# Optimization experiments

Measured on AMD Instinct MI355X. Metric: run time of the kernel, lower is better.

Reference implementation:

```python
import jax, jax.numpy as jnp
import numpy as np

DECAY = 0.8
EPS = 1e-05


def setup_inputs() -> dict:
    key = jax.random.key(0)
    k1, k2, k3 = jax.random.split(key, 3)
    b, n, d = 16, 4096, 64
    h, c = 1, 2048
    x = jax.random.normal(k1, (b, n, d), dtype=jnp.float32)
    embeddings = jax.random.normal(k2, (h, c, d), dtype=jnp.float32)
    cluster_size = jnp.ones((h, c), dtype=jnp.float32)
    embed_avg = jax.random.normal(k3, (h, c, d), dtype=jnp.float32)
    return {"x": x, "embeddings": embeddings, "cluster_size": cluster_size, "embed_avg": embed_avg}


def reference(x, embeddings, cluster_size, embed_avg):
    # x: (b, n, d); add codebook dim h=1 and flatten -> (h, N, d)
    d = x.shape[-1]
    flat = x.reshape(1, -1, d)                              # (h, N, d)
    h, C = embeddings.shape[0], embeddings.shape[1]

    # dist = -cdist(flat, embeddings)  (negative euclidean distance)
    x2 = jnp.sum(flat * flat, axis=-1, keepdims=True)       # (h, N, 1)
    e2 = jnp.sum(embeddings * embeddings, axis=-1)          # (h, C)
    xe = jnp.einsum('hnd,hcd->hnc', flat, embeddings)       # (h, N, C)
    dist = -jnp.sqrt(jnp.clip(x2 + e2[:, None, :] - 2.0 * xe, 0.0))

    # gumbel_sample with stochastic=False, straight_through=False -> hard argmax
    embed_ind = jnp.argmax(dist, axis=-1)                   # (h, N)

    # quantize: gather selected codes
    quantize = jnp.take_along_axis(embeddings, embed_ind[..., None], axis=1)  # (h, N, d)

    # EMA codebook update (scatter-based): counts and per-code feature sums
    counts = jax.vmap(lambda i: jnp.bincount(i, length=C))(embed_ind).astype(x.dtype)  # (h, C)
    embed_sum = jax.vmap(lambda f, i: jax.ops.segment_sum(f, i, num_segments=C))(flat, embed_ind)  # (h, C, d)

    new_cluster_size = cluster_size * DECAY + counts * (1.0 - DECAY)
    new_embed_avg = embed_avg * DECAY + embed_sum * (1.0 - DECAY)

    # laplace smoothing of cluster sizes, then renormalize embed_avg
    tot = jnp.sum(new_cluster_size, axis=-1, keepdims=True)
    smoothed = (new_cluster_size + EPS) / (tot + C * EPS) * tot
    new_embeddings = new_embed_avg / smoothed[..., None]

    quantize = quantize.reshape(x.shape)                    # drop h dim back to (b, n, d)
    embed_ind = embed_ind.reshape(x.shape[:-1])             # (b, n)
    return quantize, embed_ind, new_embeddings, new_cluster_size, new_embed_avg
```

## Files before the change

kernel.cpp:

```cpp
#include <hip/hip_runtime.h>

#define N_TOK 65536
#define D 64
#define C_CODES 2048
#define DECAYF 0.8f
#define OMDF 0.2f
#define EPSF 1e-5f
#define SEG 16
#define GAP_THR 0.0625f
#define TCODES 64
#define HT (1024 / TCODES)

#define OUT_QUANT 0
#define OUT_IND   (N_TOK * D)
#define OUT_EMB   (OUT_IND + N_TOK)
#define OUT_CS    (OUT_EMB + C_CODES * D)
#define OUT_EAVG  (OUT_CS + C_CODES)

typedef short s16x8 __attribute__((ext_vector_type(8)));
typedef float f32x4 __attribute__((ext_vector_type(4)));

__device__ __forceinline__ unsigned short f2bf(float f) {
    unsigned int u = __float_as_uint(f);
    return (unsigned short)((u + 0x7fffu + ((u >> 16) & 1u)) >> 16);
}
__device__ __forceinline__ float bf2f(unsigned short h) {
    return __uint_as_float(((unsigned int)h) << 16);
}
__device__ __forceinline__ unsigned long long shflx64w(unsigned long long v, int mask, int w) {
    unsigned int lo = (unsigned int)v, hi = (unsigned int)(v >> 32);
    lo = __shfl_xor(lo, mask, w);
    hi = __shfl_xor(hi, mask, w);
    return ((unsigned long long)hi << 32) | lo;
}
__device__ __forceinline__ void gload_lds16(const void* g, void* l) {
    __builtin_amdgcn_global_load_lds(
        (const __attribute__((address_space(1))) void*)g,
        (__attribute__((address_space(3))) void*)l, 16, 0, 0);
}

__global__ void eprep_kernel(const float* __restrict__ emb, short* __restrict__ ebk,
                             float* __restrict__ e2, unsigned int* __restrict__ e2p,
                             float* __restrict__ counts, float* __restrict__ embed_sum) {
    int g = blockIdx.x * blockDim.x + threadIdx.x;
    int code = g >> 3, slot = g & 7;
    int kc = slot ^ (code & 7);
    const float4* ep = (const float4*)(emb + (size_t)code * D + kc * 8);
    float4 a = ep[0], b = ep[1];
    float v[8] = {a.x, a.y, a.z, a.w, b.x, b.y, b.z, b.w};
    s16x8 h, l;
#pragma unroll
    for (int j = 0; j < 8; ++j) {
        unsigned short hb = f2bf(v[j]);
        h[j] = (short)hb;
        l[j] = (short)f2bf(v[j] - bf2f(hb));
    }
    *(s16x8*)(ebk + (size_t)code * 128 + slot * 8) = h;
    *(s16x8*)(ebk + (size_t)code * 128 + 64 + slot * 8) = l;

    float4 z = {0.f, 0.f, 0.f, 0.f};
    ((float4*)embed_sum)[g * 2] = z;
    ((float4*)embed_sum)[g * 2 + 1] = z;
    if (g < C_CODES / 4) ((float4*)counts)[g] = z;

    if (g < C_CODES) {
        const float4* er = (const float4*)(emb + (size_t)g * D);
        float s0 = 0.f, s1 = 0.f, s2 = 0.f, s3 = 0.f;
#pragma unroll
        for (int i = 0; i < D / 4; ++i) {
            float4 e = er[i];
            s0 = fmaf(e.x, e.x, s0);
            s1 = fmaf(e.y, e.y, s1);
            s2 = fmaf(e.z, e.z, s2);
            s3 = fmaf(e.w, e.w, s3);
        }
        float vv = (s0 + s1) + (s2 + s3);
        e2[g] = vv;
        unsigned short hb = f2bf(vv);
        unsigned short lb = f2bf(vv - bf2f(hb));
        e2p[g] = (unsigned int)hb | ((unsigned int)lb << 16);
    }
}

__global__ __launch_bounds__(256) void screen_kernel(
        const float* __restrict__ x, const short* __restrict__ ebk,
        const unsigned int* __restrict__ e2p, uint4* __restrict__ ktop2,
        float* __restrict__ kb3) {
    __shared__ unsigned int e2pl[1024];
    __shared__ __align__(16) char bstage[2][TCODES * 256];

    const int tid = threadIdx.x;
    const int bh = blockIdx.y;
    ((uint4*)e2pl)[tid] = ((const uint4*)(e2p + bh * 1024))[tid];

    const int lane = tid & 63;
    const int wave = tid >> 6;
    const int col = lane & 15;
    const int krow = lane >> 4;

    s16x8 ah[2][2], al[2][2];
#pragma unroll
    for (int s = 0; s < 2; ++s) {
        int tok = blockIdx.x * 128 + wave * 32 + s * 16 + col;
        const float4* xp = (const float4*)(x + (size_t)tok * D + krow * 8);
        float4 f0 = xp[0], f1 = xp[1], f2 = xp[8], f3 = xp[9];
        float xv[16] = {f0.x, f0.y, f0.z, f0.w, f1.x, f1.y, f1.z, f1.w,
                        f2.x, f2.y, f2.z, f2.w, f3.x, f3.y, f3.z, f3.w};
#pragma unroll
        for (int j = 0; j < 8; ++j) {
            float v0 = -2.0f * xv[j];
            unsigned short h0 = f2bf(v0);
            ah[s][0][j] = (short)h0;
            al[s][0][j] = (short)f2bf(v0 - bf2f(h0));
            float v1 = -2.0f * xv[8 + j];
            unsigned short h1 = f2bf(v1);
            ah[s][1][j] = (short)h1;
            al[s][1][j] = (short)f2bf(v1 - bf2f(h1));
        }
    }

    s16x8 aone = {0, 0, 0, 0, 0, 0, 0, 0};
    {
        short o = (krow == 0) ? (short)0x3F80 : (short)0;
        aone[0] = o;
        aone[1] = o;
    }
    const f32x4 zero = {0.f, 0.f, 0.f, 0.f};

    float b1[2][4], b2[2][4], b3[2][4];
    unsigned int c1[2][4], c2[2][4];
#pragma unroll
    for (int s = 0; s < 2; ++s)
#pragma unroll
        for (int r = 0; r < 4; ++r) {
            b1[s][r] = __builtin_inff();
            b2[s][r] = __builtin_inff();
            b3[s][r] = __builtin_inff();
            c1[s][r] = 0u;
            c2[s][r] = 0u;
        }

    auto stage = [&](int b, int t) {
        const char* src = (const char*)ebk + (size_t)(bh * HT + t) * (TCODES * 256)
                          + wave * 4096 + lane * 16;
        char* dst = &bstage[b][wave * 4096];
        gload_lds16(src, dst);
        gload_lds16(src + 1024, dst + 1024);
        gload_lds16(src + 2048, dst + 2048);
        gload_lds16(src + 3072, dst + 3072);
    };

    auto subtile = [&](const char* lb, int t, int j) {
        const char* base = lb + (j << 12) + (col << 8);
        int off = (krow ^ (col & 7)) << 4;
        s16x8 bh0 = *(const s16x8*)(base + off);
        s16x8 bh1 = *(const s16x8*)(base + (off ^ 64));
        s16x8 bl0 = *(const s16x8*)(base + 128 + off);
        s16x8 bl1 = *(const s16x8*)(base + 128 + (off ^ 64));
        int sloc = t * 4 + j;
        unsigned int cg = (unsigned int)(bh * 1024 + sloc * 16 + col);
        unsigned int v = e2pl[sloc * 16 + col];
        v = (krow == 0) ? v : 0u;
        s16x8 be2 = {(short)(v & 0xffffu), (short)(v >> 16), 0, 0, 0, 0, 0, 0};
        f32x4 f = __builtin_amdgcn_mfma_f32_16x16x32_bf16(aone, be2, zero, 0, 0, 0);
#pragma unroll
        for (int s = 0; s < 2; ++s) {
            f32x4 acc = __builtin_amdgcn_mfma_f32_16x16x32_bf16(ah[s][1], bh1, f, 0, 0, 0);
            acc = __builtin_amdgcn_mfma_f32_16x16x32_bf16(ah[s][0], bh0, acc, 0, 0, 0);
            acc = __builtin_amdgcn_mfma_f32_16x16x32_bf16(al[s][1], bh1, acc, 0, 0, 0);
            acc = __builtin_amdgcn_mfma_f32_16x16x32_bf16(al[s][0], bh0, acc, 0, 0, 0);
            acc = __builtin_amdgcn_mfma_f32_16x16x32_bf16(ah[s][1], bl1, acc, 0, 0, 0);
            acc = __builtin_amdgcn_mfma_f32_16x16x32_bf16(ah[s][0], bl0, acc, 0, 0, 0);
#pragma unroll
            for (int r = 0; r < 4; ++r) {
                float sc = acc[r];
                bool l1 = sc < b1[s][r];
                bool l2 = sc < b2[s][r];
                b3[s][r] = __builtin_amdgcn_fmed3f(b2[s][r], b3[s][r], sc);
                b2[s][r] = __builtin_amdgcn_fmed3f(b1[s][r], b2[s][r], sc);
                unsigned int tc = l1 ? c1[s][r] : cg;
                c2[s][r] = l2 ? tc : c2[s][r];
                b1[s][r] = fminf(b1[s][r], sc);
                c1[s][r] = l1 ? cg : c1[s][r];
            }
        }
    };

    stage(0, 0);
    __syncthreads();

    for (int t = 0; t < HT; ++t) {
        if (t + 1 < HT) stage((t + 1) & 1, t + 1);
        const char* lb = bstage[t & 1];
        subtile(lb, t, 0);
        subtile(lb, t, 1);
        subtile(lb, t, 2);
        subtile(lb, t, 3);
        __syncthreads();
    }

#pragma unroll
    for (int s = 0; s < 2; ++s)
#pragma unroll
        for (int r = 0; r < 4; ++r) {
            float B1 = b1[s][r], B2 = b2[s][r], B3 = b3[s][r];
            unsigned int C1 = c1[s][r], C2 = c2[s][r];
#pragma unroll
            for (int mk = 1; mk < 16; mk <<= 1) {
                float o1 = __shfl_xor(B1, mk, 16);
                float o2 = __shfl_xor(B2, mk, 16);
                float o3 = __shfl_xor(B3, mk, 16);
                unsigned int oc1 = (unsigned int)__shfl_xor((int)C1, mk, 16);
                unsigned int oc2 = (unsigned int)__shfl_xor((int)C2, mk, 16);
                bool ta = B1 <= o1;
                float x1v = ta ? o1 : B1;
                unsigned int xc = ta ? oc1 : C1;
                float nm1 = ta ? B1 : o1;
                unsigned int nc1 = ta ? C1 : oc1;
                bool tb = B2 <= o2;
                float y1v = tb ? B2 : o2;
                unsigned int yc = tb ? C2 : oc2;
                bool tc = x1v <= y1v;
                float nm2 = tc ? x1v : y1v;
                unsigned int nc2 = tc ? xc : yc;
                float nm3 = fminf(fmaxf(x1v, y1v), fminf(B3, o3));
                B1 = nm1; C1 = nc1; B2 = nm2; C2 = nc2; B3 = nm3;
            }
            if (col == 0) {
                int tok = blockIdx.x * 128 + wave * 32 + s * 16 + krow * 4 + r;
                uint4 o;
                o.x = __float_as_uint(B1);
                o.y = C1;
                o.z = __float_as_uint(B2);
                o.w = C2;
                ktop2[(size_t)tok * 2 + bh] = o;
                kb3[(size_t)tok * 2 + bh] = B3;
            }
        }
}

__global__ __launch_bounds__(256) void exact_kernel(
        const float* __restrict__ x, const float* __restrict__ emb,
        const float* __restrict__ e2, const uint4* __restrict__ ktop2,
        const float* __restrict__ kb3,
        int* __restrict__ idx, float* __restrict__ out,
        float* __restrict__ counts) {
    __shared__ float lcount[C_CODES];
    for (int i = threadIdx.x; i < C_CODES; i += blockDim.x) lcount[i] = 0.0f;
    __syncthreads();
    int n = blockIdx.x * blockDim.x + threadIdx.x;
    int lane = threadIdx.x & 63;

    uint4 A = ktop2[(size_t)n * 2];
    uint4 B = ktop2[(size_t)n * 2 + 1];
    float a3 = kb3[(size_t)n * 2], b3v = kb3[(size_t)n * 2 + 1];
    float a1 = __uint_as_float(A.x), a2 = __uint_as_float(A.z);
    float b1f = __uint_as_float(B.x), b2f = __uint_as_float(B.z);

    bool ta = a1 <= b1f;
    float m1 = ta ? a1 : b1f;
    int cm1 = (int)(ta ? A.y : B.y);
    float x1v = ta ? b1f : a1;
    int xc = (int)(ta ? B.y : A.y);
    bool tb = a2 <= b2f;
    float y1v = tb ? a2 : b2f;
    int yc = (int)(tb ? A.w : B.w);
    bool tc = x1v <= y1v;
    float m2 = tc ? x1v : y1v;
    int cm2 = tc ? xc : yc;
    float m3 = fminf(fmaxf(x1v, y1v), fminf(a3, b3v));

    int c = cm1;
    bool uniq = (m2 - m1 > GAP_THR);
    bool pairf = !uniq && (m3 - m1 > GAP_THR);
    bool fullf = !uniq && !pairf;

    if (pairf) {
        int ca = cm1, cb = cm2;
        float xs[4] = {0.f, 0.f, 0.f, 0.f};
        float da[4] = {0.f, 0.f, 0.f, 0.f};
        float db[4] = {0.f, 0.f, 0.f, 0.f};
        for (int q = 0; q < 4; ++q) {
            const float4* xq = (const float4*)(x + (size_t)n * D + q * 16);
            const float4* ea = (const float4*)(emb + (size_t)ca * D + q * 16);
            const float4* eb = (const float4*)(emb + (size_t)cb * D + q * 16);
#pragma unroll
            for (int j = 0; j < 4; ++j) {
                float4 xv = xq[j], av = ea[j], bv = eb[j];
                xs[0] = fmaf(xv.x, xv.x, xs[0]);
                xs[1] = fmaf(xv.y, xv.y, xs[1]);
                xs[2] = fmaf(xv.z, xv.z, xs[2]);
                xs[3] = fmaf(xv.w, xv.w, xs[3]);
                da[0] = fmaf(xv.x, av.x, da[0]);
                da[1] = fmaf(xv.y, av.y, da[1]);
                da[2] = fmaf(xv.z, av.z, da[2]);
                da[3] = fmaf(xv.w, av.w, da[3]);
                db[0] = fmaf(xv.x, bv.x, db[0]);
                db[1] = fmaf(xv.y, bv.y, db[1]);
                db[2] = fmaf(xv.z, bv.z, db[2]);
                db[3] = fmaf(xv.w, bv.w, db[3]);
            }
        }
        float x2 = (xs[0] + xs[1]) + (xs[2] + xs[3]);
        float dota = (da[0] + da[1]) + (da[2] + da[3]);
        float dA = fmaxf(x2 + e2[ca] - 2.0f * dota, 0.0f);
        float dotb = (db[0] + db[1]) + (db[2] + db[3]);
        float dB = fmaxf(x2 + e2[cb] - 2.0f * dotb, 0.0f);
        unsigned long long ka = ((unsigned long long)__float_as_uint(dA) << 32) | (unsigned int)ca;
        unsigned long long kb = ((unsigned long long)__float_as_uint(dB) << 32) | (unsigned int)cb;
        c = (int)((ka < kb ? ka : kb) & 0xffffffffull);
    }

    unsigned long long bal = __ballot(fullf);
    while (bal) {
        int src = (int)__ffsll((long long)bal) - 1;
        bal &= bal - 1;
        int tn = (n & ~63) + src;
        float xs[4] = {0.f, 0.f, 0.f, 0.f};
        for (int q = 0; q < 4; ++q) {
            const float4* xq = (const float4*)(x + (size_t)tn * D + q * 16);
#pragma unroll
            for (int j = 0; j < 4; ++j) {
                float4 xv = xq[j];
                xs[0] = fmaf(xv.x, xv.x, xs[0]);
                xs[1] = fmaf(xv.y, xv.y, xs[1]);
                xs[2] = fmaf(xv.z, xv.z, xs[2]);
                xs[3] = fmaf(xv.w, xv.w, xs[3]);
            }
        }
        float tx2 = (xs[0] + xs[1]) + (xs[2] + xs[3]);
        unsigned long long kbest = ~0ull;
        for (int cc = lane; cc < C_CODES; cc += 64) {
            float d0 = 0.f, d1 = 0.f, d2 = 0.f, d3 = 0.f;
            for (int q = 0; q < 4; ++q) {
                const float4* xq = (const float4*)(x + (size_t)tn * D + q * 16);
                const float4* er = (const float4*)(emb + (size_t)cc * D + q * 16);
#pragma unroll
                for (int j = 0; j < 4; ++j) {
                    float4 xv = xq[j], ev = er[j];
                    d0 = fmaf(xv.x, ev.x, d0);
                    d1 = fmaf(xv.y, ev.y, d1);
                    d2 = fmaf(xv.z, ev.z, d2);
                    d3 = fmaf(xv.w, ev.w, d3);
                }
            }
            float dot = (d0 + d1) + (d2 + d3);
            float dist2 = fmaxf(tx2 + e2[cc] - 2.0f * dot, 0.0f);
            unsigned long long key =
                ((unsigned long long)__float_as_uint(dist2) << 32) | (unsigned int)cc;
            kbest = key < kbest ? key : kbest;
        }
#pragma unroll
        for (int mk = 1; mk < 64; mk <<= 1) {
            unsigned long long o = shflx64w(kbest, mk, 64);
            kbest = o < kbest ? o : kbest;
        }
        if (lane == src) c = (int)(kbest & 0xffffffffull);
    }

    idx[n] = c;
    out[OUT_IND + n] = (float)c;
    atomicAdd(&lcount[c], 1.0f);

    {
        const float4* er = (const float4*)(emb + (size_t)c * D);
        float4* qo = (float4*)(out + OUT_QUANT) + (size_t)n * 16;
#pragma unroll
        for (int q = 0; q < 16; ++q) qo[q] = er[q];
    }

    __syncthreads();
    for (int i = threadIdx.x; i < C_CODES; i += blockDim.x) {
        float vv = lcount[i];
        if (vv != 0.0f) atomicAdd(&counts[i], vv);
    }
}

__global__ void prefix_ema_kernel(const float* __restrict__ counts,
                                  const float* __restrict__ cluster_size,
                                  float* __restrict__ out,
                                  float* __restrict__ smoothed,
                                  int* __restrict__ cursor) {
    __shared__ float scan[256];
    __shared__ float red[256];
    int t = threadIdx.x;
    int base = t * 8;
    float cnt[8], ncs[8];
    float csum = 0.f, nsum = 0.f;
#pragma unroll
    for (int j = 0; j < 8; ++j) {
        cnt[j] = counts[base + j];
        csum += cnt[j];
        ncs[j] = cluster_size[base + j] * DECAYF + cnt[j] * OMDF;
        nsum += ncs[j];
        out[OUT_CS + base + j] = ncs[j];
    }
    scan[t] = csum;
    red[t] = nsum;
    __syncthreads();
    for (int s = 1; s < 256; s <<= 1) {
        float v = scan[t];
        float w = (t >= s) ? scan[t - s] : 0.f;
        __syncthreads();
        scan[t] = v + w;
        __syncthreads();
    }
    for (int s = 128; s > 0; s >>= 1) {
        if (t < s) red[t] += red[t + s];
        __syncthreads();
    }
    float tot = red[0];
    float run = (t == 0) ? 0.f : scan[t - 1];
#pragma unroll
    for (int j = 0; j < 8; ++j) {
        cursor[base + j] = (int)run;
        run += cnt[j];
        smoothed[base + j] = (ncs[j] + EPSF) / (tot + (float)C_CODES * EPSF) * tot;
    }
}

__global__ void scatter_pos_kernel(const int* __restrict__ idx,
                                   int* __restrict__ cursor,
                                   unsigned int* __restrict__ sorted) {
    int n = blockIdx.x * blockDim.x + threadIdx.x;
    int c = idx[n];
    int pos = atomicAdd(&cursor[c], 1);
    sorted[pos] = ((unsigned int)c << 16) | (unsigned int)n;
}

__global__ __launch_bounds__(256) void seg_sum_kernel(
        const float* __restrict__ x, const unsigned int* __restrict__ sorted,
        float* __restrict__ embed_sum) {
    int lane = threadIdx.x & 63;
    int q = blockIdx.x * 4 + (threadIdx.x >> 6);
    int p0 = q * SEG;

    unsigned int mine = (lane < SEG) ? sorted[p0 + lane] : 0u;
    unsigned int pk[SEG];
#pragma unroll
    for (int j = 0; j < SEG; ++j) pk[j] = __shfl(mine, j, 64);

    float xv[SEG];
#pragma unroll
    for (int j = 0; j < SEG; ++j)
        xv[j] = x[(size_t)(pk[j] & 0xffffu) * D + lane];

    unsigned int run_c = 0xffffffffu;
    float sum = 0.f;
#pragma unroll
    for (int j = 0; j < SEG; ++j) {
        unsigned int c = pk[j] >> 16;
        if (c != run_c) {
            if (run_c != 0xffffffffu)
                atomicAdd(&embed_sum[(size_t)run_c * D + lane], sum);
            run_c = c;
            sum = 0.f;
        }
        sum += xv[j];
    }
    atomicAdd(&embed_sum[(size_t)run_c * D + lane], sum);
}

__global__ void ema_embed_kernel(const float* __restrict__ embed_avg,
                                 const float* __restrict__ embed_sum,
                                 const float* __restrict__ smoothed,
                                 float* __restrict__ out) {
    int g = blockIdx.x * blockDim.x + threadIdx.x;
    int c = g >> 4;
    float4 ea = ((const float4*)embed_avg)[g];
    float4 es = ((const float4*)embed_sum)[g];
    float4 na;
    na.x = ea.x * DECAYF + es.x * OMDF;
    na.y = ea.y * DECAYF + es.y * OMDF;
    na.z = ea.z * DECAYF + es.z * OMDF;
    na.w = ea.w * DECAYF + es.w * OMDF;
    ((float4*)(out + OUT_EAVG))[g] = na;
    float sm = smoothed[c];
    float4 ne;
    ne.x = na.x / sm;
    ne.y = na.y / sm;
    ne.z = na.z / sm;
    ne.w = na.w / sm;
    ((float4*)(out + OUT_EMB))[g] = ne;
}

extern "C" void kernel_launch(void* const* d_in, const int* in_sizes, int n_in,
                              void* d_out, int out_size, void* d_ws, size_t ws_size,
                              hipStream_t stream) {
    const float* x            = (const float*)d_in[0];
    const float* emb          = (const float*)d_in[1];
    const float* cluster_size = (const float*)d_in[2];
    const float* embed_avg    = (const float*)d_in[3];
    float* out = (float*)d_out;

    float* e2        = (float*)d_ws;
    unsigned int* e2p = (unsigned int*)(e2 + C_CODES);
    float* counts    = (float*)(e2p + C_CODES);
    float* smoothed  = counts + C_CODES;
    int*   cursor    = (int*)(smoothed + C_CODES);
    int*   idx       = cursor + C_CODES;
    unsigned int* sorted = (unsigned int*)(idx + N_TOK);
    uint4* ktop2     = (uint4*)(sorted + N_TOK);
    float* kb3       = (float*)(ktop2 + (size_t)N_TOK * 2);
    float* embed_sum = kb3 + (size_t)N_TOK * 2;
    short* ebk       = (short*)(embed_sum + C_CODES * D);

    eprep_kernel<<<(C_CODES * 8) / 256, 256, 0, stream>>>(emb, ebk, e2, e2p, counts, embed_sum);
    screen_kernel<<<dim3(N_TOK / 128, 2), 256, 0, stream>>>(x, ebk, e2p, ktop2, kb3);
    exact_kernel<<<N_TOK / 256, 256, 0, stream>>>(x, emb, e2, ktop2, kb3, idx, out, counts);
    prefix_ema_kernel<<<1, 256, 0, stream>>>(counts, cluster_size, out, smoothed, cursor);
    scatter_pos_kernel<<<N_TOK / 256, 256, 0, stream>>>(idx, cursor, sorted);
    seg_sum_kernel<<<(N_TOK / SEG) / 4, 256, 0, stream>>>(x, sorted, embed_sum);
    ema_embed_kernel<<<(C_CODES * 16) / 256, 256, 0, stream>>>(embed_avg, embed_sum,
                                                              smoothed, out);
}
```

Before: 249.6 us.

## Scan full codebook per block and compact ambiguous tokens into cleanup queue

The screen kernel now scans all 2048 codes in one block instead of splitting the codebook across two grid halves. This removes the ktop2/kb3 merge buffers, and the kernel resolves unique or pair cases in place, writing idx and counts directly. Tokens that need a full exact search are appended to a global pending list, which a fixed-size cleanup kernel processes with one wave per token. This replaces the ballot loop that stalled whole waves. The quantize gather moves to a separate coalesced kernel. The screen grid is halved, so there is less parallelism per launch, and global atomics on counts replace the shared-memory histogram.

```diff
diff --git a/kernel.cpp b/kernel.cpp
--- a/kernel.cpp
+++ b/kernel.cpp
@@ -9,7 +9,7 @@
 #define SEG 16
 #define GAP_THR 0.0625f
 #define TCODES 64
-#define HT (1024 / TCODES)
+#define NTILES (C_CODES / TCODES)
 
 #define OUT_QUANT 0
 #define OUT_IND   (N_TOK * D)
@@ -41,7 +41,8 @@
 
 __global__ void eprep_kernel(const float* __restrict__ emb, short* __restrict__ ebk,
                              float* __restrict__ e2, unsigned int* __restrict__ e2p,
-                             float* __restrict__ counts, float* __restrict__ embed_sum) {
+                             float* __restrict__ counts, float* __restrict__ embed_sum,
+                             int* __restrict__ pend_n) {
     int g = blockIdx.x * blockDim.x + threadIdx.x;
     int code = g >> 3, slot = g & 7;
     int kc = slot ^ (code & 7);
@@ -62,6 +63,7 @@
     ((float4*)embed_sum)[g * 2] = z;
     ((float4*)embed_sum)[g * 2 + 1] = z;
     if (g < C_CODES / 4) ((float4*)counts)[g] = z;
+    if (g == 0) pend_n[0] = 0;
 
     if (g < C_CODES) {
         const float4* er = (const float4*)(emb + (size_t)g * D);
@@ -83,15 +85,18 @@
 }
 
 __global__ __launch_bounds__(256) void screen_kernel(
-        const float* __restrict__ x, const short* __restrict__ ebk,
-        const unsigned int* __restrict__ e2p, uint4* __restrict__ ktop2,
-        float* __restrict__ kb3) {
-    __shared__ unsigned int e2pl[1024];
+        const float* __restrict__ x, const float* __restrict__ emb,
+        const short* __restrict__ ebk, const float* __restrict__ e2,
+        const unsigned int* __restrict__ e2p,
+        int* __restrict__ idx, float* __restrict__ out, float* __restrict__ counts,
+        int* __restrict__ pend_n, unsigned int* __restrict__ pend) {
+    __shared__ unsigned int e2pl[C_CODES];
     __shared__ __align__(16) char bstage[2][TCODES * 256];
+    __shared__ unsigned int fin[4][32][5];
 
     const int tid = threadIdx.x;
-    const int bh = blockIdx.y;
-    ((uint4*)e2pl)[tid] = ((const uint4*)(e2p + bh * 1024))[tid];
+    ((uint4*)e2pl)[tid] = ((const uint4*)e2p)[tid];
+    ((uint4*)e2pl)[tid + 256] = ((const uint4*)e2p)[tid + 256];
 
     const int lane = tid & 63;
     const int wave = tid >> 6;
@@ -141,7 +146,7 @@
         }
 
     auto stage = [&](int b, int t) {
-        const char* src = (const char*)ebk + (size_t)(bh * HT + t) * (TCODES * 256)
+        const char* src = (const char*)ebk + (size_t)t * (TCODES * 256)
                           + wave * 4096 + lane * 16;
         char* dst = &bstage[b][wave * 4096];
         gload_lds16(src, dst);
@@ -158,7 +163,7 @@
         s16x8 bl0 = *(const s16x8*)(base + 128 + off);
         s16x8 bl1 = *(const s16x8*)(base + 128 + (off ^ 64));
         int sloc = t * 4 + j;
-        unsigned int cg = (unsigned int)(bh * 1024 + sloc * 16 + col);
+        unsigned int cg = (unsigned int)(sloc * 16 + col);
         unsigned int v = e2pl[sloc * 16 + col];
         v = (krow == 0) ? v : 0u;
         s16x8 be2 = {(short)(v & 0xffffu), (short)(v >> 16), 0, 0, 0, 0, 0, 0};
@@ -189,8 +194,8 @@
     stage(0, 0);
     __syncthreads();
 
-    for (int t = 0; t < HT; ++t) {
-        if (t + 1 < HT) stage((t + 1) & 1, t + 1);
+    for (int t = 0; t < NTILES; ++t) {
+        if (t + 1 < NTILES) stage((t + 1) & 1, t + 1);
         const char* lb = bstage[t & 1];
         subtile(lb, t, 0);
         subtile(lb, t, 1);
@@ -227,95 +232,88 @@
                 B1 = nm1; C1 = nc1; B2 = nm2; C2 = nc2; B3 = nm3;
             }
             if (col == 0) {
-                int tok = blockIdx.x * 128 + wave * 32 + s * 16 + krow * 4 + r;
-                uint4 o;
-                o.x = __float_as_uint(B1);
-                o.y = C1;
-                o.z = __float_as_uint(B2);
-                o.w = C2;
-                ktop2[(size_t)tok * 2 + bh] = o;
-                kb3[(size_t)tok * 2 + bh] = B3;
+                int tl = s * 16 + krow * 4 + r;
+                fin[wave][tl][0] = __float_as_uint(B1);
+                fin[wave][tl][1] = C1;
+                fin[wave][tl][2] = __float_as_uint(B2);
+                fin[wave][tl][3] = C2;
+                fin[wave][tl][4] = __float_as_uint(B3);
             }
         }
-}
-
-__global__ __launch_bounds__(256) void exact_kernel(
+    __syncthreads();
+
+    if (lane < 32) {
+        const unsigned int* f = fin[wave][lane];
+        float m1 = __uint_as_float(f[0]);
+        int cm1 = (int)f[1];
+        float m2 = __uint_as_float(f[2]);
+        int cm2 = (int)f[3];
+        float m3 = __uint_as_float(f[4]);
+        int tok = blockIdx.x * 128 + wave * 32 + lane;
+        bool uniq = (m2 - m1 > GAP_THR);
+        bool pairf = !uniq && (m3 - m1 > GAP_THR);
+        int c = cm1;
+
+        if (pairf) {
+            int ca = cm1, cb = cm2;
+            float xs[4] = {0.f, 0.f, 0.f, 0.f};
+            float da[4] = {0.f, 0.f, 0.f, 0.f};
+            float db[4] = {0.f, 0.f, 0.f, 0.f};
+            for (int q = 0; q < 4; ++q) {
+                const float4* xq = (const float4*)(x + (size_t)tok * D + q * 16);
+                const float4* ea = (const float4*)(emb + (size_t)ca * D + q * 16);
+                const float4* eb = (const float4*)(emb + (size_t)cb * D + q * 16);
+#pragma unroll
+                for (int j = 0; j < 4; ++j) {
+                    float4 xv = xq[j], av = ea[j], bv = eb[j];
+                    xs[0] = fmaf(xv.x, xv.x, xs[0]);
+                    xs[1] = fmaf(xv.y, xv.y, xs[1]);
+                    xs[2] = fmaf(xv.z, xv.z, xs[2]);
+                    xs[3] = fmaf(xv.w, xv.w, xs[3]);
+                    da[0] = fmaf(xv.x, av.x, da[0]);
+                    da[1] = fmaf(xv.y, av.y, da[1]);
+                    da[2] = fmaf(xv.z, av.z, da[2]);
+                    da[3] = fmaf(xv.w, av.w, da[3]);
+                    db[0] = fmaf(xv.x, bv.x, db[0]);
+                    db[1] = fmaf(xv.y, bv.y, db[1]);
+                    db[2] = fmaf(xv.z, bv.z, db[2]);
+                    db[3] = fmaf(xv.w, bv.w, db[3]);
+                }
+            }
+            float x2 = (xs[0] + xs[1]) + (xs[2] + xs[3]);
+            float dota = (da[0] + da[1]) + (da[2] + da[3]);
+            float dA = fmaxf(x2 + e2[ca] - 2.0f * dota, 0.0f);
+            float dotb = (db[0] + db[1]) + (db[2] + db[3]);
+            float dB = fmaxf(x2 + e2[cb] - 2.0f * dotb, 0.0f);
+            unsigned long long ka =
+                ((unsigned long long)__float_as_uint(dA) << 32) | (unsigned int)ca;
+            unsigned long long kb =
+                ((unsigned long long)__float_as_uint(dB) << 32) | (unsigned int)cb;
+            c = (int)((ka < kb ? ka : kb) & 0xffffffffull);
+        }
+
+        if (uniq || pairf) {
+            idx[tok] = c;
+            out[OUT_IND + tok] = (float)c;
+            atomicAdd(&counts[c], 1.0f);
+        } else {
+            int p = atomicAdd(pend_n, 1);
+            pend[p] = (unsigned int)tok;
+        }
+    }
+}
+
+__global__ __launch_bounds__(256) void cleanup_kernel(
         const float* __restrict__ x, const float* __restrict__ emb,
-        const float* __restrict__ e2, const uint4* __restrict__ ktop2,
-        const float* __restrict__ kb3,
-        int* __restrict__ idx, float* __restrict__ out,
-        float* __restrict__ counts) {
-    __shared__ float lcount[C_CODES];
-    for (int i = threadIdx.x; i < C_CODES; i += blockDim.x) lcount[i] = 0.0f;
-    __syncthreads();
-    int n = blockIdx.x * blockDim.x + threadIdx.x;
+        const float* __restrict__ e2, const int* __restrict__ pend_n,
+        const unsigned int* __restrict__ pend,
+        int* __restrict__ idx, float* __restrict__ out, float* __restrict__ counts) {
+    int gw = (int)((blockIdx.x * blockDim.x + threadIdx.x) >> 6);
+    int nw = (int)((gridDim.x * blockDim.x) >> 6);
     int lane = threadIdx.x & 63;
-
-    uint4 A = ktop2[(size_t)n * 2];
-    uint4 B = ktop2[(size_t)n * 2 + 1];
-    float a3 = kb3[(size_t)n * 2], b3v = kb3[(size_t)n * 2 + 1];
-    float a1 = __uint_as_float(A.x), a2 = __uint_as_float(A.z);
-    float b1f = __uint_as_float(B.x), b2f = __uint_as_float(B.z);
-
-    bool ta = a1 <= b1f;
-    float m1 = ta ? a1 : b1f;
-    int cm1 = (int)(ta ? A.y : B.y);
-    float x1v = ta ? b1f : a1;
-    int xc = (int)(ta ? B.y : A.y);
-    bool tb = a2 <= b2f;
-    float y1v = tb ? a2 : b2f;
-    int yc = (int)(tb ? A.w : B.w);
-    bool tc = x1v <= y1v;
-    float m2 = tc ? x1v : y1v;
-    int cm2 = tc ? xc : yc;
-    float m3 = fminf(fmaxf(x1v, y1v), fminf(a3, b3v));
-
-    int c = cm1;
-    bool uniq = (m2 - m1 > GAP_THR);
-    bool pairf = !uniq && (m3 - m1 > GAP_THR);
-    bool fullf = !uniq && !pairf;
-
-    if (pairf) {
-        int ca = cm1, cb = cm2;
-        float xs[4] = {0.f, 0.f, 0.f, 0.f};
-        float da[4] = {0.f, 0.f, 0.f, 0.f};
-        float db[4] = {0.f, 0.f, 0.f, 0.f};
-        for (int q = 0; q < 4; ++q) {
-            const float4* xq = (const float4*)(x + (size_t)n * D + q * 16);
-            const float4* ea = (const float4*)(emb + (size_t)ca * D + q * 16);
-            const float4* eb = (const float4*)(emb + (size_t)cb * D + q * 16);
-#pragma unroll
-            for (int j = 0; j < 4; ++j) {
-                float4 xv = xq[j], av = ea[j], bv = eb[j];
-                xs[0] = fmaf(xv.x, xv.x, xs[0]);
-                xs[1] = fmaf(xv.y, xv.y, xs[1]);
-                xs[2] = fmaf(xv.z, xv.z, xs[2]);
-                xs[3] = fmaf(xv.w, xv.w, xs[3]);
-                da[0] = fmaf(xv.x, av.x, da[0]);
-                da[1] = fmaf(xv.y, av.y, da[1]);
-                da[2] = fmaf(xv.z, av.z, da[2]);
-                da[3] = fmaf(xv.w, av.w, da[3]);
-                db[0] = fmaf(xv.x, bv.x, db[0]);
-                db[1] = fmaf(xv.y, bv.y, db[1]);
-                db[2] = fmaf(xv.z, bv.z, db[2]);
-                db[3] = fmaf(xv.w, bv.w, db[3]);
-            }
-        }
-        float x2 = (xs[0] + xs[1]) + (xs[2] + xs[3]);
-        float dota = (da[0] + da[1]) + (da[2] + da[3]);
-        float dA = fmaxf(x2 + e2[ca] - 2.0f * dota, 0.0f);
-        float dotb = (db[0] + db[1]) + (db[2] + db[3]);
-        float dB = fmaxf(x2 + e2[cb] - 2.0f * dotb, 0.0f);
-        unsigned long long ka = ((unsigned long long)__float_as_uint(dA) << 32) | (unsigned int)ca;
-        unsigned long long kb = ((unsigned long long)__float_as_uint(dB) << 32) | (unsigned int)cb;
-        c = (int)((ka < kb ? ka : kb) & 0xffffffffull);
-    }
-
-    unsigned long long bal = __ballot(fullf);
-    while (bal) {
-        int src = (int)__ffsll((long long)bal) - 1;
-        bal &= bal - 1;
-        int tn = (n & ~63) + src;
+    int M = pend_n[0];
+    for (int i = gw; i < M; i += nw) {
+        int tn = (int)pend[i];
         float xs[4] = {0.f, 0.f, 0.f, 0.f};
         for (int q = 0; q < 4; ++q) {
             const float4* xq = (const float4*)(x + (size_t)tn * D + q * 16);
@@ -355,25 +353,24 @@
             unsigned long long o = shflx64w(kbest, mk, 64);
             kbest = o < kbest ? o : kbest;
         }
-        if (lane == src) c = (int)(kbest & 0xffffffffull);
-    }
-
-    idx[n] = c;
-    out[OUT_IND + n] = (float)c;
-    atomicAdd(&lcount[c], 1.0f);
-
-    {
-        const float4* er = (const float4*)(emb + (size_t)c * D);
-        float4* qo = (float4*)(out + OUT_QUANT) + (size_t)n * 16;
-#pragma unroll
-        for (int q = 0; q < 16; ++q) qo[q] = er[q];
-    }
-
-    __syncthreads();
-    for (int i = threadIdx.x; i < C_CODES; i += blockDim.x) {
-        float vv = lcount[i];
-        if (vv != 0.0f) atomicAdd(&counts[i], vv);
-    }
+        if (lane == 0) {
+            int c = (int)(kbest & 0xffffffffull);
+            idx[tn] = c;
+            out[OUT_IND + tn] = (float)c;
+            atomicAdd(&counts[c], 1.0f);
+        }
+    }
+}
+
+__global__ void gather_kernel(const float* __restrict__ emb,
+                              const int* __restrict__ idx,
+                              float* __restrict__ out) {
+    int g = blockIdx.x * blockDim.x + threadIdx.x;
+    int n = g >> 4;
+    int j = g & 15;
+    int c = idx[n];
+    float4 e = ((const float4*)emb)[c * (D / 4) + j];
+    ((float4*)(out + OUT_QUANT))[g] = e;
 }
 
 __global__ void prefix_ema_kernel(const float* __restrict__ counts,
@@ -500,14 +497,17 @@
     int*   cursor    = (int*)(smoothed + C_CODES);
     int*   idx       = cursor + C_CODES;
     unsigned int* sorted = (unsigned int*)(idx + N_TOK);
-    uint4* ktop2     = (uint4*)(sorted + N_TOK);
-    float* kb3       = (float*)(ktop2 + (size_t)N_TOK * 2);
-    float* embed_sum = kb3 + (size_t)N_TOK * 2;
+    int*   pend_n    = (int*)(sorted + N_TOK);
+    unsigned int* pend = (unsigned int*)(pend_n + 4);
+    float* embed_sum = (float*)(pend + N_TOK);
     short* ebk       = (short*)(embed_sum + C_CODES * D);
 
-    eprep_kernel<<<(C_CODES * 8) / 256, 256, 0, stream>>>(emb, ebk, e2, e2p, counts, embed_sum);
-    screen_kernel<<<dim3(N_TOK / 128, 2), 256, 0, stream>>>(x, ebk, e2p, ktop2, kb3);
-    exact_kernel<<<N_TOK / 256, 256, 0, stream>>>(x, emb, e2, ktop2, kb3, idx, out, counts);
+    eprep_kernel<<<(C_CODES * 8) / 256, 256, 0, stream>>>(emb, ebk, e2, e2p, counts,
+                                                          embed_sum, pend_n);
+    screen_kernel<<<N_TOK / 128, 256, 0, stream>>>(x, emb, ebk, e2, e2p, idx, out,
+                                                   counts, pend_n, pend);
+    cleanup_kernel<<<128, 256, 0, stream>>>(x, emb, e2, pend_n, pend, idx, out, counts);
+    gather_kernel<<<(N_TOK * 16) / 256, 256, 0, stream>>>(emb, idx, out);
     prefix_ema_kernel<<<1, 256, 0, stream>>>(counts, cluster_size, out, smoothed, cursor);
     scatter_pos_kernel<<<N_TOK / 256, 256, 0, stream>>>(idx, cursor, sorted);
     seg_sum_kernel<<<(N_TOK / SEG) / 4, 256, 0, stream>>>(x, sorted, embed_sum);
```

New measurement: 270.9 us. 8.5% more time.
